# Optimization experiments

Hardware: AMD Instinct MI355X
Metric: run time of the kernel (lower is better)

Reference implementation:

```python
import jax, jax.numpy as jnp
import numpy as np

ROWS, COLS = 4096, 11008          # out_features, in_features
NCB, CBSIZE, CLEN = 2, 256, 8     # num_codebooks, 2**nbits, in_group_size
RANK = 32
BLOCK = ROWS                      # bolck_size = reference_weight.shape[0]
N_CODES = ROWS * COLS // CLEN     # total number of codebook entries gathered


def setup_inputs() -> dict:
    key = jax.random.key(0)
    k1, k2, k3, k4, k5 = jax.random.split(key, 5)
    codebooks = jax.random.normal(k1, (NCB, CBSIZE, CLEN), dtype=jnp.float32)
    codes = jax.random.randint(k2, (NCB, N_CODES // NCB), 0, CBSIZE, dtype=jnp.int32)
    scales = jax.random.uniform(k3, (COLS, 1), dtype=jnp.float32, minval=0.5, maxval=1.5)
    L = jax.random.normal(k4, (ROWS, RANK), dtype=jnp.float32) * 0.02
    R = jax.random.normal(k5, (RANK, COLS), dtype=jnp.float32) * 0.02
    return {"codebooks": codebooks, "codes": codes, "scales": scales, "L": L, "R": R}


def reference(codebooks, codes, scales, L, R):
    # differentiable_dequantize: per-codebook gather (embedding_bag with 1-elem
    # bags == plain gather), then per-block scale, then reshape back to weight.
    gathered = jax.vmap(lambda cb, c: cb[c])(codebooks, codes)  # (NCB, N/NCB, CLEN)
    blocks = gathered.reshape(-1, BLOCK) * scales               # (COLS, ROWS) * (COLS,1)
    dequant = blocks.reshape(ROWS, COLS)
    # low-rank correction
    return dequant + L @ R
```

## Files before the change

kernel.cpp:

```cpp
#include <hip/hip_runtime.h>

constexpr int kRows  = 4096;
constexpr int kCols  = 11008;
constexpr int kRank  = 32;
constexpr int kHalfF = 22544384;

constexpr int RT    = 32;
constexpr int CT    = 256;
constexpr int PITCH = 260;

typedef __attribute__((ext_vector_type(8))) short short8;
typedef __attribute__((ext_vector_type(4))) float f32x4;

__device__ __forceinline__ unsigned short bf16_rne(float x) {
    union { float f; unsigned u; } v; v.f = x;
    return (unsigned short)((v.u + 0x7FFFu + ((v.u >> 16) & 1u)) >> 16);
}

__global__ __launch_bounds__(256) void prep(
    const float* __restrict__ Lm,
    const float* __restrict__ Rm,
    unsigned short* __restrict__ Lb,
    unsigned short* __restrict__ Rbt)
{
    const int tid = threadIdx.x;
    const int b   = blockIdx.x;
    if (b < 43) {
        const int j = b * 256 + tid;
        #pragma unroll
        for (int t = 0; t < 4; ++t) {
            short8 o;
            #pragma unroll
            for (int k = 0; k < 8; ++k)
                o[k] = (short)bf16_rne(Rm[(t * 8 + k) * kCols + j]);
            *(short8*)(Rbt + j * kRank + t * 8) = o;
        }
    } else {
        const int t0 = ((b - 43) * 256 + tid) * 8;
        const float4 a0 = *(const float4*)(Lm + t0);
        const float4 a1 = *(const float4*)(Lm + t0 + 4);
        short8 o;
        o[0] = (short)bf16_rne(a0.x); o[1] = (short)bf16_rne(a0.y);
        o[2] = (short)bf16_rne(a0.z); o[3] = (short)bf16_rne(a0.w);
        o[4] = (short)bf16_rne(a1.x); o[5] = (short)bf16_rne(a1.y);
        o[6] = (short)bf16_rne(a1.z); o[7] = (short)bf16_rne(a1.w);
        *(short8*)(Lb + t0) = o;
    }
}

__global__ __launch_bounds__(256) void qw_fused(
    const float* __restrict__ codebooks,
    const int*   __restrict__ codes,
    const float* __restrict__ scales,
    const unsigned short* __restrict__ Lb,
    const unsigned short* __restrict__ Rbt,
    float* __restrict__ outp)
{
    __shared__ __attribute__((aligned(16))) float cb_lds[2 * 256 * 8];
    __shared__ __attribute__((aligned(16))) float corr[RT * PITCH];

    const int tid = threadIdx.x;
    const int i0 = blockIdx.y * RT;
    const int j0 = blockIdx.x * CT;

    {
        const float4* src = (const float4*)codebooks;
        float4* dst = (float4*)cb_lds;
        #pragma unroll
        for (int t = 0; t < 4; ++t) dst[tid + t * 256] = src[tid + t * 256];
    }

    {
        const int wave = tid >> 6;
        const int lane = tid & 63;
        const int n16  = lane & 15;
        const int q    = lane >> 4;

        const short8 af = *(const short8*)(Lb + (i0 + ((wave & 1) << 4) + n16) * kRank + (q << 3));

        const unsigned short* bbase =
            Rbt + (size_t)(j0 + ((wave >> 1) << 7) + n16) * kRank + (q << 3);
        short8 bf[8];
        #pragma unroll
        for (int nt = 0; nt < 8; ++nt)
            bf[nt] = *(const short8*)(bbase + nt * 16 * kRank);

        const int row_base = ((wave & 1) << 4) + (q << 2);
        const int cbase    = ((wave >> 1) << 7) + n16;

        #pragma unroll
        for (int nt = 0; nt < 8; ++nt) {
            f32x4 acc = {0.f, 0.f, 0.f, 0.f};
            acc = __builtin_amdgcn_mfma_f32_16x16x32_bf16(af, bf[nt], acc, 0, 0, 0);
            const int ccol = cbase + nt * 16;
            #pragma unroll
            for (int r = 0; r < 4; ++r)
                corr[(row_base + r) * PITCH + ccol] = acc[r];
        }
    }

    __syncthreads();

    {
        const int lane4 = (tid & 63) << 2;
        const int rbase = tid >> 6;
        #pragma unroll
        for (int p = 0; p < 8; ++p) {
            const int row = rbase + (p << 2);
            const int f = (i0 + row) * kCols + j0 + lane4;
            const int code = codes[f >> 3];
            const int cb   = (f >= kHalfF) ? 1 : 0;
            const float scale = scales[f >> 12];
            const float4 w = *(const float4*)(cb_lds + (cb << 11) + (code << 3) + (lane4 & 4));
            const float4 c = *(const float4*)(corr + row * PITCH + lane4);
            float4 o;
            o.x = w.x * scale + c.x;
            o.y = w.y * scale + c.y;
            o.z = w.z * scale + c.z;
            o.w = w.w * scale + c.w;
            *(float4*)(outp + f) = o;
        }
    }
}

extern "C" void kernel_launch(void* const* d_in, const int* in_sizes, int n_in,
                              void* d_out, int out_size, void* d_ws, size_t ws_size,
                              hipStream_t stream) {
    const float* codebooks = (const float*)d_in[0];
    const int*   codes     = (const int*)d_in[1];
    const float* scales    = (const float*)d_in[2];
    const float* Lm        = (const float*)d_in[3];
    const float* Rm        = (const float*)d_in[4];
    float* outp            = (float*)d_out;

    unsigned short* Lb  = (unsigned short*)d_ws;
    unsigned short* Rbt = Lb + kRows * kRank;

    prep<<<dim3(43 + 64), dim3(256), 0, stream>>>(Lm, Rm, Lb, Rbt);

    dim3 grid(kCols / CT, kRows / RT);
    qw_fused<<<grid, dim3(256), 0, stream>>>(codebooks, codes, scales, Lb, Rbt, outp);
}
```

Measured before the change: 217.1 us.

## Fuse low-rank MFMA result directly into dequant epilogue, drop LDS staging

Swaps the MFMA operands so each lane's accumulator holds four consecutive columns of one output row. The epilogue can then add the correction straight from registers, and the shared-memory correction tile with its store/load round trip is removed. Codebook selection becomes a per-block constant based on row half. The cost is that stores now cover 16-byte chunks at 64-byte stride per lane within a row, across 16 rows per wave, so global write coalescing is less contiguous than the previous row-major float4 layout.

New measurement: 233.8 us. 1.08x slower.

```diff
diff --git a/kernel.cpp b/kernel.cpp
--- a/kernel.cpp
+++ b/kernel.cpp
@@ -3,11 +3,9 @@
 constexpr int kRows  = 4096;
 constexpr int kCols  = 11008;
 constexpr int kRank  = 32;
-constexpr int kHalfF = 22544384;
 
-constexpr int RT    = 32;
-constexpr int CT    = 256;
-constexpr int PITCH = 260;
+constexpr int RT = 32;
+constexpr int CT = 256;
 
 typedef __attribute__((ext_vector_type(8))) short short8;
 typedef __attribute__((ext_vector_type(4))) float f32x4;
@@ -57,11 +55,24 @@
     float* __restrict__ outp)
 {
     __shared__ __attribute__((aligned(16))) float cb_lds[2 * 256 * 8];
-    __shared__ __attribute__((aligned(16))) float corr[RT * PITCH];
 
-    const int tid = threadIdx.x;
+    const int tid  = threadIdx.x;
+    const int wave = tid >> 6;
+    const int lane = tid & 63;
+    const int n16  = lane & 15;
+    const int q    = lane >> 4;
     const int i0 = blockIdx.y * RT;
     const int j0 = blockIdx.x * CT;
+
+    const short8 lf = *(const short8*)(
+        Lb + (size_t)(i0 + ((wave & 1) << 4) + n16) * kRank + (q << 3));
+
+    const unsigned short* rbase =
+        Rbt + (size_t)(j0 + ((wave >> 1) << 7) + n16) * kRank + (q << 3);
+    short8 rf[8];
+    #pragma unroll
+    for (int nt = 0; nt < 8; ++nt)
+        rf[nt] = *(const short8*)(rbase + nt * 16 * kRank);
 
     {
         const float4* src = (const float4*)codebooks;
@@ -69,57 +80,28 @@
         #pragma unroll
         for (int t = 0; t < 4; ++t) dst[tid + t * 256] = src[tid + t * 256];
     }
-
-    {
-        const int wave = tid >> 6;
-        const int lane = tid & 63;
-        const int n16  = lane & 15;
-        const int q    = lane >> 4;
-
-        const short8 af = *(const short8*)(Lb + (i0 + ((wave & 1) << 4) + n16) * kRank + (q << 3));
-
-        const unsigned short* bbase =
-            Rbt + (size_t)(j0 + ((wave >> 1) << 7) + n16) * kRank + (q << 3);
-        short8 bf[8];
-        #pragma unroll
-        for (int nt = 0; nt < 8; ++nt)
-            bf[nt] = *(const short8*)(bbase + nt * 16 * kRank);
-
-        const int row_base = ((wave & 1) << 4) + (q << 2);
-        const int cbase    = ((wave >> 1) << 7) + n16;
-
-        #pragma unroll
-        for (int nt = 0; nt < 8; ++nt) {
-            f32x4 acc = {0.f, 0.f, 0.f, 0.f};
-            acc = __builtin_amdgcn_mfma_f32_16x16x32_bf16(af, bf[nt], acc, 0, 0, 0);
-            const int ccol = cbase + nt * 16;
-            #pragma unroll
-            for (int r = 0; r < 4; ++r)
-                corr[(row_base + r) * PITCH + ccol] = acc[r];
-        }
-    }
-
     __syncthreads();
 
-    {
-        const int lane4 = (tid & 63) << 2;
-        const int rbase = tid >> 6;
-        #pragma unroll
-        for (int p = 0; p < 8; ++p) {
-            const int row = rbase + (p << 2);
-            const int f = (i0 + row) * kCols + j0 + lane4;
-            const int code = codes[f >> 3];
-            const int cb   = (f >= kHalfF) ? 1 : 0;
-            const float scale = scales[f >> 12];
-            const float4 w = *(const float4*)(cb_lds + (cb << 11) + (code << 3) + (lane4 & 4));
-            const float4 c = *(const float4*)(corr + row * PITCH + lane4);
-            float4 o;
-            o.x = w.x * scale + c.x;
-            o.y = w.y * scale + c.y;
-            o.z = w.z * scale + c.z;
-            o.w = w.w * scale + c.w;
-            *(float4*)(outp + f) = o;
-        }
+    const int row     = i0 + ((wave & 1) << 4) + n16;
+    const int colbase = j0 + ((wave >> 1) << 7) + (q << 2);
+    const int fbase   = row * kCols + colbase;
+    const float* cbp = cb_lds + ((i0 >= (kRows >> 1)) ? 2048 : 0) + ((q & 1) << 2);
+
+    #pragma unroll
+    for (int nt = 0; nt < 8; ++nt) {
+        f32x4 acc = {0.f, 0.f, 0.f, 0.f};
+        acc = __builtin_amdgcn_mfma_f32_16x16x32_bf16(rf[nt], lf, acc, 0, 0, 0);
+
+        const int f     = fbase + nt * 16;
+        const int code  = codes[f >> 3];
+        const float scale = scales[f >> 12];
+        const float4 w  = *(const float4*)(cbp + (code << 3));
+        float4 o;
+        o.x = w.x * scale + acc[0];
+        o.y = w.y * scale + acc[1];
+        o.z = w.z * scale + acc[2];
+        o.w = w.w * scale + acc[3];
+        *(float4*)(outp + f) = o;
     }
 }
 
```

## Halve row tile, load one codebook per block, use nontemporal output stores

Applied to the files above, without the earlier changes.

Row tile shrinks from 32 to 16, so each block computes a 16x256 low-rank correction with four MFMAs per wave and uses less LDS. Each block now loads only the codebook for its half of the rows, since a 16-row tile never straddles the codebook boundary. Launch bounds request 6 blocks per SIMD and output stores become nontemporal to avoid cache pollution. The aim is higher occupancy and less LDS traffic in a store-bound kernel, at the cost of twice as many blocks, each repeating the codebook staging and the L/R operand fetches.

Result: slower. 223.0 us (+2.7%).

```diff
diff --git a/kernel.cpp b/kernel.cpp
--- a/kernel.cpp
+++ b/kernel.cpp
@@ -3,9 +3,8 @@
 constexpr int kRows  = 4096;
 constexpr int kCols  = 11008;
 constexpr int kRank  = 32;
-constexpr int kHalfF = 22544384;
 
-constexpr int RT    = 32;
+constexpr int RT    = 16;
 constexpr int CT    = 256;
 constexpr int PITCH = 260;
 
@@ -48,7 +47,7 @@
     }
 }
 
-__global__ __launch_bounds__(256) void qw_fused(
+__global__ __launch_bounds__(256, 6) void qw_fused(
     const float* __restrict__ codebooks,
     const int*   __restrict__ codes,
     const float* __restrict__ scales,
@@ -56,7 +55,7 @@
     const unsigned short* __restrict__ Rbt,
     float* __restrict__ outp)
 {
-    __shared__ __attribute__((aligned(16))) float cb_lds[2 * 256 * 8];
+    __shared__ __attribute__((aligned(16))) float cb_lds[256 * 8];
     __shared__ __attribute__((aligned(16))) float corr[RT * PITCH];
 
     const int tid = threadIdx.x;
@@ -64,10 +63,11 @@
     const int j0 = blockIdx.x * CT;
 
     {
-        const float4* src = (const float4*)codebooks;
-        float4* dst = (float4*)cb_lds;
+        const int sel = (i0 >= (kRows >> 1)) ? 1 : 0;
+        const f32x4* src = (const f32x4*)codebooks + (sel << 9);
+        f32x4* dst = (f32x4*)cb_lds;
         #pragma unroll
-        for (int t = 0; t < 4; ++t) dst[tid + t * 256] = src[tid + t * 256];
+        for (int t = 0; t < 2; ++t) dst[tid + t * 256] = src[tid + t * 256];
     }
 
     {
@@ -76,22 +76,22 @@
         const int n16  = lane & 15;
         const int q    = lane >> 4;
 
-        const short8 af = *(const short8*)(Lb + (i0 + ((wave & 1) << 4) + n16) * kRank + (q << 3));
+        const short8 af = *(const short8*)(Lb + (size_t)(i0 + n16) * kRank + (q << 3));
 
         const unsigned short* bbase =
-            Rbt + (size_t)(j0 + ((wave >> 1) << 7) + n16) * kRank + (q << 3);
-        short8 bf[8];
+            Rbt + (size_t)(j0 + (wave << 6) + n16) * kRank + (q << 3);
+        short8 bfr[4];
         #pragma unroll
-        for (int nt = 0; nt < 8; ++nt)
-            bf[nt] = *(const short8*)(bbase + nt * 16 * kRank);
+        for (int nt = 0; nt < 4; ++nt)
+            bfr[nt] = *(const short8*)(bbase + nt * 16 * kRank);
 
-        const int row_base = ((wave & 1) << 4) + (q << 2);
-        const int cbase    = ((wave >> 1) << 7) + n16;
+        const int row_base = q << 2;
+        const int cbase    = (wave << 6) + n16;
 
         #pragma unroll
-        for (int nt = 0; nt < 8; ++nt) {
+        for (int nt = 0; nt < 4; ++nt) {
             f32x4 acc = {0.f, 0.f, 0.f, 0.f};
-            acc = __builtin_amdgcn_mfma_f32_16x16x32_bf16(af, bf[nt], acc, 0, 0, 0);
+            acc = __builtin_amdgcn_mfma_f32_16x16x32_bf16(af, bfr[nt], acc, 0, 0, 0);
             const int ccol = cbase + nt * 16;
             #pragma unroll
             for (int r = 0; r < 4; ++r)
@@ -105,20 +105,19 @@
         const int lane4 = (tid & 63) << 2;
         const int rbase = tid >> 6;
         #pragma unroll
-        for (int p = 0; p < 8; ++p) {
+        for (int p = 0; p < 4; ++p) {
             const int row = rbase + (p << 2);
             const int f = (i0 + row) * kCols + j0 + lane4;
             const int code = codes[f >> 3];
-            const int cb   = (f >= kHalfF) ? 1 : 0;
             const float scale = scales[f >> 12];
-            const float4 w = *(const float4*)(cb_lds + (cb << 11) + (code << 3) + (lane4 & 4));
-            const float4 c = *(const float4*)(corr + row * PITCH + lane4);
-            float4 o;
-            o.x = w.x * scale + c.x;
-            o.y = w.y * scale + c.y;
-            o.z = w.z * scale + c.z;
-            o.w = w.w * scale + c.w;
-            *(float4*)(outp + f) = o;
+            const f32x4 w = *(const f32x4*)(cb_lds + (code << 3) + (lane4 & 4));
+            const f32x4 c = *(const f32x4*)(corr + row * PITCH + lane4);
+            f32x4 o;
+            o[0] = w[0] * scale + c[0];
+            o[1] = w[1] * scale + c[1];
+            o[2] = w[2] * scale + c[2];
+            o[3] = w[3] * scale + c[3];
+            __builtin_nontemporal_store(o, (f32x4*)(outp + f));
         }
     }
 }
```
